# Kernel tuning notes

Measured on AMD Instinct MI355X. Metric: run time of the kernel, lower is better.

## Reference

```python
import jax, jax.numpy as jnp
import numpy as np

ANCHOR_LENGTHS = jnp.array([1., 2., 3., 4., 5., 7., 9.], dtype=jnp.float32)  # A = 7


def make_anchors_1d(Lf):
    # anchors [Lf*A, 2] in feature coords, matching torch make_anchors_1d
    centers = jnp.arange(Lf, dtype=jnp.float32) + 0.5          # [Lf]
    c = centers[:, None]                                        # [Lf,1]
    w = ANCHOR_LENGTHS[None, :]                                 # [1,A]
    start = c - 0.5 * w
    end = c + 0.5 * w
    return jnp.stack(jnp.broadcast_arrays(start, end), axis=-1).reshape(-1, 2)


def setup_inputs() -> dict:
    key = jax.random.key(0)
    ks = jax.random.split(key, 4)
    B, C, Lf, A = 8, 512, 16384, 7
    feat = jax.random.normal(ks[0], (B, C, Lf), dtype=jnp.float32)
    conv_w = jax.random.normal(ks[1], (C, C, 3), dtype=jnp.float32) * 0.02
    conv_b = jnp.zeros((C,), dtype=jnp.float32)
    obj_w = jax.random.normal(ks[2], (A, C, 1), dtype=jnp.float32) * 0.02
    obj_b = jnp.zeros((A,), dtype=jnp.float32)
    reg_w = jax.random.normal(ks[3], (A * 2, C, 1), dtype=jnp.float32) * 0.02
    reg_b = jnp.zeros((A * 2,), dtype=jnp.float32)
    return {"feat": feat, "conv_w": conv_w, "conv_b": conv_b,
            "obj_w": obj_w, "obj_b": obj_b, "reg_w": reg_w, "reg_b": reg_b}


def reference(feat, conv_w, conv_b, obj_w, obj_b, reg_w, reg_b):
    B, C, Lf = feat.shape
    A = obj_w.shape[0]
    # conv1d k=3 pad=1 (NCH layout), + bias, relu
    h = jax.lax.conv_general_dilated(
        feat, conv_w, window_strides=(1,), padding=((1, 1),),
        dimension_numbers=("NCH", "OIH", "NCH"))
    h = jax.nn.relu(h + conv_b[None, :, None])                  # [B,C,Lf]
    # 1x1 heads as channel contractions
    obj = jnp.einsum("bcl,ac->bla", h, obj_w[:, :, 0]) + obj_b  # [B,Lf,A]
    reg = jnp.einsum("bcl,oc->blo", h, reg_w[:, :, 0]) + reg_b  # [B,Lf,2A]
    obj = obj.reshape(B, Lf * A)                                # [B,N]
    reg = reg.reshape(B, Lf, A, 2).reshape(B, Lf * A, 2)        # [B,N,2]
    anchors = make_anchors_1d(Lf)                               # [N,2]
    return obj, reg, anchors
```

## Files before the change

### kernel.cpp

```cpp
#include <hip/hip_runtime.h>
#include <hip/hip_bf16.h>
#include <stdint.h>

typedef __attribute__((ext_vector_type(4))) float f32x4;
typedef __attribute__((ext_vector_type(16))) float f32x16;
typedef __attribute__((ext_vector_type(4))) int i32x4;
typedef __attribute__((ext_vector_type(8))) int i32x8;
typedef __attribute__((ext_vector_type(8))) short bh8;
typedef unsigned short u16;
typedef unsigned int u32;
typedef unsigned char u8;

#define B_    8
#define C_    512
#define LF    16384
#define KTOT  1536
#define SCL   0x7F7F7F7Fu

#define P4_BYTES ((size_t)4 * B_ * 21 * LF * 4)
#define W8_OFF   P4_BYTES

#define OBJ_OFF  0
#define REG_OFF  917504
#define ANC_OFF  2752512

__device__ __forceinline__ u16 f2bf(float f) {
    u32 u = __float_as_uint(f);
    return (u16)((u + 0x7FFFu + ((u >> 16) & 1u)) >> 16);
}
__device__ __forceinline__ u32 pk2bf(float lo, float hi) {
    u32 r;
    asm("v_cvt_pk_bf16_f32 %0, %1, %2" : "=v"(r) : "v"(lo), "v"(hi));
    return r;
}
__device__ __forceinline__ void gload16(const u8* g, u8* l) {
    __builtin_amdgcn_global_load_lds(
        (const __attribute__((address_space(1))) void*)g,
        (__attribute__((address_space(3))) void*)l, 16, 0, 0);
}

__global__ void k_cast_w(const float* __restrict__ cw, u8* __restrict__ W8) {
    int i = blockIdx.x * 256 + threadIdx.x;
    if (i >= C_ * KTOT / 2) return;
    int co = i / (KTOT / 2);
    int rr = (i % (KTOT / 2)) * 2;
    int t = rr / 512, q = rr % 512;
    int kc = q >> 6, cc = q & 63;
    int jl = (cc >> 4) ^ ((co >> 1) & 3);
    int ci = kc * 64 + jl * 16 + (cc & 15);
    float f0 = cw[(co * C_ + ci) * 3 + t];
    float f1 = cw[(co * C_ + ci + 1) * 3 + t];
    u32 pk = __builtin_amdgcn_cvt_pk_fp8_f32(f0, f1, 0, false);
    *(u16*)&W8[(size_t)co * KTOT + rr] = (u16)pk;
}

__global__ void k_anchors(float* __restrict__ out) {
    int l = blockIdx.x * 256 + threadIdx.x;
    if (l >= LF) return;
    const float AL[7] = {1.f, 2.f, 3.f, 4.f, 5.f, 7.f, 9.f};
    float c = (float)l + 0.5f;
    float* an = out + ANC_OFF + (size_t)l * 14;
#pragma unroll
    for (int a = 0; a < 7; ++a) {
        an[a * 2 + 0] = c - 0.5f * AL[a];
        an[a * 2 + 1] = c + 0.5f * AL[a];
    }
}

__global__ __launch_bounds__(256, 2) void k_conv_head(
    const float* __restrict__ feat, const u8* __restrict__ W8,
    const float* __restrict__ conv_b, const float* __restrict__ obj_w,
    const float* __restrict__ reg_w, float* __restrict__ P4) {
    __shared__ __align__(16) char smem[40960];
    u8* As3 = (u8*)smem;
    u8* Bs  = (u8*)(smem + 24576);
    u16* Hs = (u16*)smem;
    u16* Wp = (u16*)(smem + 32768);

    const int tid = threadIdx.x;
    const int lane = tid & 63, wave = tid >> 6;
    const int wm = wave >> 1, wn = wave & 1;
    const int g = lane >> 4, cL = lane & 15;
    const int r32 = lane & 31, hK = lane >> 5;

    const int wg = (blockIdx.x & 7) * 512 + (blockIdx.x >> 3);
    const int mt = wg & 3;
    const int l0 = ((wg >> 2) & 127) * 128;
    const int b  = wg >> 9;
    const int co0 = mt * 128;

    const int cg = tid & 15, lgrp = tid >> 4;

    f32x16 acc[2][2];
#pragma unroll
    for (int mi = 0; mi < 2; ++mi)
#pragma unroll
        for (int ni = 0; ni < 2; ++ni)
#pragma unroll
            for (int r = 0; r < 16; ++r) acc[mi][ni][r] = 0.f;

    for (int kc = 0; kc < 8; ++kc) {
        __syncthreads();
        {
            const float* fp = feat +
                ((size_t)(b * C_ + kc * 64 + cg * 4)) * LF + l0 + lgrp * 8;
            const int slog = cg >> 2;
            const int soff = (cg * 4) & 15;
#pragma unroll
            for (int h = 0; h < 2; ++h) {
                float4 v0 = *(const float4*)(fp + 0 * LF + h * 4);
                float4 v1 = *(const float4*)(fp + 1 * LF + h * 4);
                float4 v2 = *(const float4*)(fp + 2 * LF + h * 4);
                float4 v3 = *(const float4*)(fp + 3 * LF + h * 4);
#pragma unroll
                for (int e = 0; e < 4; ++e) {
                    const int r = 1 + lgrp * 8 + h * 4 + e;
                    u32 w0 = __builtin_amdgcn_cvt_pk_fp8_f32(
                        ((const float*)&v0)[e], ((const float*)&v1)[e], 0, false);
                    u32 w  = __builtin_amdgcn_cvt_pk_fp8_f32(
                        ((const float*)&v2)[e], ((const float*)&v3)[e], w0, true);
                    const int pc = ((slog ^ ((r >> 1) & 3)) * 16) + soff;
                    *(u32*)&Bs[r * 64 + pc] = w;
                }
            }
        }
        if (tid < 128) {
            const int ci2 = tid >> 1;
            const int rr = (tid & 1) ? 129 : 0;
            const int l = l0 + ((tid & 1) ? 128 : -1);
            float v = (l >= 0 && l < LF)
                          ? feat[((size_t)(b * C_ + kc * 64 + ci2)) * LF + l]
                          : 0.f;
            u32 p = __builtin_amdgcn_cvt_pk_fp8_f32(v, 0.f, 0, false);
            const int pc = (((ci2 >> 4) ^ ((rr >> 1) & 3)) * 16) + (ci2 & 15);
            Bs[rr * 64 + pc] = (u8)p;
        }
#pragma unroll
        for (int t = 0; t < 3; ++t)
#pragma unroll
            for (int p = 0; p < 2; ++p) {
                const int row = p * 64 + (tid >> 2);
                const int colB = (tid & 3) * 16;
                gload16(&W8[(size_t)(co0 + row) * KTOT + t * 512 + kc * 64 + colB],
                        &As3[t * 8192 + row * 64 + colB]);
            }
        __syncthreads();
#pragma unroll
        for (int t = 0; t < 3; ++t) {
            const u8* At = As3 + t * 8192;
            i32x8 af[2], bf[2];
#pragma unroll
            for (int mi = 0; mi < 2; ++mi) {
                const int row = wm * 64 + mi * 32 + r32;
                const int x = (row >> 1) & 3;
                i32x4 a0 = *(const i32x4*)&At[row * 64 + (((2 * hK) ^ x) * 16)];
                i32x4 a1 = *(const i32x4*)&At[row * 64 + (((2 * hK + 1) ^ x) * 16)];
                af[mi] = __builtin_shufflevector(a0, a1, 0, 1, 2, 3, 4, 5, 6, 7);
            }
#pragma unroll
            for (int ni = 0; ni < 2; ++ni) {
                const int row = wn * 64 + ni * 32 + r32 + t;
                const int x = (row >> 1) & 3;
                i32x4 b0 = *(const i32x4*)&Bs[row * 64 + (((2 * hK) ^ x) * 16)];
                i32x4 b1 = *(const i32x4*)&Bs[row * 64 + (((2 * hK + 1) ^ x) * 16)];
                bf[ni] = __builtin_shufflevector(b0, b1, 0, 1, 2, 3, 4, 5, 6, 7);
            }
#pragma unroll
            for (int mi = 0; mi < 2; ++mi)
#pragma unroll
                for (int ni = 0; ni < 2; ++ni)
                    acc[mi][ni] = __builtin_amdgcn_mfma_scale_f32_32x32x64_f8f6f4(
                        af[mi], bf[ni], acc[mi][ni], 0, 0, 0, SCL, 0, SCL);
        }
    }
    __syncthreads();

#pragma unroll
    for (int mi = 0; mi < 2; ++mi)
#pragma unroll
        for (int ni = 0; ni < 2; ++ni) {
            const int l_loc = wn * 64 + ni * 32 + r32;
            const int xw = (l_loc & 7) << 3;
#pragma unroll
            for (int q = 0; q < 4; ++q) {
                const int cb = wm * 64 + mi * 32 + q * 8 + 4 * hK;
                const float b0_ = conv_b[co0 + cb + 0];
                const float b1_ = conv_b[co0 + cb + 1];
                const float b2_ = conv_b[co0 + cb + 2];
                const float b3_ = conv_b[co0 + cb + 3];
                uint2 pk;
                pk.x = pk2bf(fmaxf(acc[mi][ni][q * 4 + 0] + b0_, 0.f),
                             fmaxf(acc[mi][ni][q * 4 + 1] + b1_, 0.f));
                pk.y = pk2bf(fmaxf(acc[mi][ni][q * 4 + 2] + b2_, 0.f),
                             fmaxf(acc[mi][ni][q * 4 + 3] + b3_, 0.f));
                *(uint2*)&Hs[l_loc * 128 + (cb ^ xw)] = pk;
            }
        }
#pragma unroll
    for (int it = 0; it < 4; ++it) {
        const int q = it * 256 + tid;
        const int a = q >> 5, c0 = (q & 31) * 4;
        float4 wv = {0.f, 0.f, 0.f, 0.f};
        if (a < 7)       wv = *(const float4*)&obj_w[a * C_ + co0 + c0];
        else if (a < 21) wv = *(const float4*)&reg_w[(a - 7) * C_ + co0 + c0];
        uint2 pk;
        pk.x = pk2bf(wv.x, wv.y);
        pk.y = pk2bf(wv.z, wv.w);
        *(uint2*)&Wp[a * 128 + (c0 ^ ((a & 7) << 3))] = pk;
    }
    __syncthreads();

    f32x4 hacc[2][2];
#pragma unroll
    for (int m = 0; m < 2; ++m)
#pragma unroll
        for (int n = 0; n < 2; ++n) hacc[m][n] = {0.f, 0.f, 0.f, 0.f};
    const int ln0 = wave * 32;
    const int swA = (cL & 7) << 3;
#pragma unroll
    for (int ks2 = 0; ks2 < 4; ++ks2) {
        const int ko = ks2 * 32 + g * 8;
        bh8 wa[2], hb[2];
        wa[0] = *(const bh8*)&Wp[cL * 128 + (ko ^ swA)];
        wa[1] = *(const bh8*)&Wp[(16 + cL) * 128 + (ko ^ swA)];
        hb[0] = *(const bh8*)&Hs[(ln0 + cL) * 128 + (ko ^ swA)];
        hb[1] = *(const bh8*)&Hs[(ln0 + 16 + cL) * 128 + (ko ^ swA)];
#pragma unroll
        for (int m = 0; m < 2; ++m)
#pragma unroll
            for (int n = 0; n < 2; ++n)
                hacc[m][n] = __builtin_amdgcn_mfma_f32_16x16x32_bf16(
                    wa[m], hb[n], hacc[m][n], 0, 0, 0);
    }
    float* P4base = P4 + ((size_t)(mt * B_ + b) * 21) * LF + l0;
#pragma unroll
    for (int m = 0; m < 2; ++m) {
        const int a0 = m * 16 + g * 4;
#pragma unroll
        for (int n = 0; n < 2; ++n) {
            const int l = ln0 + n * 16 + cL;
#pragma unroll
            for (int r = 0; r < 4; ++r) {
                const int a = a0 + r;
                if (a < 21) P4base[(size_t)a * LF + l] = hacc[m][n][r];
            }
        }
    }
}

__global__ void k_finalize(const float* __restrict__ P4, const float* __restrict__ obj_b,
                           const float* __restrict__ reg_b, float* __restrict__ out) {
    int gid = blockIdx.x * 256 + threadIdx.x;
    if (gid >= B_ * LF) return;
    int b = gid >> 14, l = gid & (LF - 1);
    float s[21];
#pragma unroll
    for (int a = 0; a < 21; ++a) {
        float v = 0.f;
#pragma unroll
        for (int m = 0; m < 4; ++m) v += P4[((size_t)(m * B_ + b) * 21 + a) * LF + l];
        s[a] = v;
    }
    float* op = out + OBJ_OFF + (size_t)b * (LF * 7) + (size_t)l * 7;
#pragma unroll
    for (int a = 0; a < 7; ++a) op[a] = s[a] + obj_b[a];
    float* rp = out + REG_OFF + (size_t)b * (LF * 14) + (size_t)l * 14;
#pragma unroll
    for (int o = 0; o < 14; ++o) rp[o] = s[7 + o] + reg_b[o];
}

extern "C" void kernel_launch(void* const* d_in, const int* in_sizes, int n_in,
                              void* d_out, int out_size, void* d_ws, size_t ws_size,
                              hipStream_t stream) {
    const float* feat   = (const float*)d_in[0];
    const float* conv_w = (const float*)d_in[1];
    const float* conv_b = (const float*)d_in[2];
    const float* obj_w  = (const float*)d_in[3];
    const float* obj_b  = (const float*)d_in[4];
    const float* reg_w  = (const float*)d_in[5];
    const float* reg_b  = (const float*)d_in[6];
    char* ws = (char*)d_ws;
    float* P4 = (float*)ws;
    u8* W8    = (u8*)(ws + W8_OFF);
    float* out = (float*)d_out;

    k_cast_w<<<1536, 256, 0, stream>>>(conv_w, W8);
    k_anchors<<<64, 256, 0, stream>>>(out);
    k_conv_head<<<4096, 256, 0, stream>>>(feat, W8, conv_b, obj_w, reg_w, P4);
    k_finalize<<<(B_ * LF + 255) / 256, 256, 0, stream>>>(P4, obj_b, reg_b, out);
}
```

Baseline: 236.7 us.

## Double K-chunk to 128 channels, stage one tap of weights at a time, raise occupancy

The conv GEMM main loop now processes 128 input channels per outer step instead of 64, with the weight layout and XOR swizzle widened to 128-byte rows (8-way swizzle). Weights are staged one kernel tap at a time into a single 16KB buffer rather than all three taps at once, and launch bounds go from 2 to 4 blocks per CU. The aim is fewer outer iterations and higher occupancy to hide latency, at the cost of more barriers per channel chunk and heavier register use from eight float4 feature loads at a time.

```diff
diff --git a/kernel.cpp b/kernel.cpp
--- a/kernel.cpp
+++ b/kernel.cpp
@@ -24,10 +24,6 @@
 #define REG_OFF  917504
 #define ANC_OFF  2752512
 
-__device__ __forceinline__ u16 f2bf(float f) {
-    u32 u = __float_as_uint(f);
-    return (u16)((u + 0x7FFFu + ((u >> 16) & 1u)) >> 16);
-}
 __device__ __forceinline__ u32 pk2bf(float lo, float hi) {
     u32 r;
     asm("v_cvt_pk_bf16_f32 %0, %1, %2" : "=v"(r) : "v"(lo), "v"(hi));
@@ -38,6 +34,7 @@
         (const __attribute__((address_space(1))) void*)g,
         (__attribute__((address_space(3))) void*)l, 16, 0, 0);
 }
+__device__ __forceinline__ int xr7(int r) { return (r & 7) ^ ((r >> 3) & 7); }
 
 __global__ void k_cast_w(const float* __restrict__ cw, u8* __restrict__ W8) {
     int i = blockIdx.x * 256 + threadIdx.x;
@@ -45,9 +42,10 @@
     int co = i / (KTOT / 2);
     int rr = (i % (KTOT / 2)) * 2;
     int t = rr / 512, q = rr % 512;
-    int kc = q >> 6, cc = q & 63;
-    int jl = (cc >> 4) ^ ((co >> 1) & 3);
-    int ci = kc * 64 + jl * 16 + (cc & 15);
+    int kcp = q >> 7, pb = q & 127;
+    int sp = pb >> 4;
+    int sl = sp ^ xr7(co);
+    int ci = kcp * 128 + sl * 16 + (pb & 15);
     float f0 = cw[(co * C_ + ci) * 3 + t];
     float f1 = cw[(co * C_ + ci + 1) * 3 + t];
     u32 pk = __builtin_amdgcn_cvt_pk_fp8_f32(f0, f1, 0, false);
@@ -67,13 +65,13 @@
     }
 }
 
-__global__ __launch_bounds__(256, 2) void k_conv_head(
+__global__ __launch_bounds__(256, 4) void k_conv_head(
     const float* __restrict__ feat, const u8* __restrict__ W8,
     const float* __restrict__ conv_b, const float* __restrict__ obj_w,
     const float* __restrict__ reg_w, float* __restrict__ P4) {
     __shared__ __align__(16) char smem[40960];
-    u8* As3 = (u8*)smem;
-    u8* Bs  = (u8*)(smem + 24576);
+    u8* As = (u8*)smem;
+    u8* Bs = (u8*)(smem + 16384);
     u16* Hs = (u16*)smem;
     u16* Wp = (u16*)(smem + 32768);
 
@@ -99,81 +97,85 @@
 #pragma unroll
             for (int r = 0; r < 16; ++r) acc[mi][ni][r] = 0.f;
 
-    for (int kc = 0; kc < 8; ++kc) {
-        __syncthreads();
+    for (int kcp = 0; kcp < 4; ++kcp) {
         {
             const float* fp = feat +
-                ((size_t)(b * C_ + kc * 64 + cg * 4)) * LF + l0 + lgrp * 8;
-            const int slog = cg >> 2;
-            const int soff = (cg * 4) & 15;
+                ((size_t)(b * C_ + kcp * 128 + cg * 8)) * LF + l0 + lgrp * 8;
+            const int sl = cg >> 1;
+            const int half = (cg & 1) * 8;
 #pragma unroll
             for (int h = 0; h < 2; ++h) {
-                float4 v0 = *(const float4*)(fp + 0 * LF + h * 4);
-                float4 v1 = *(const float4*)(fp + 1 * LF + h * 4);
-                float4 v2 = *(const float4*)(fp + 2 * LF + h * 4);
-                float4 v3 = *(const float4*)(fp + 3 * LF + h * 4);
+                float4 v[8];
+#pragma unroll
+                for (int j = 0; j < 8; ++j)
+                    v[j] = *(const float4*)(fp + (size_t)j * LF + h * 4);
 #pragma unroll
                 for (int e = 0; e < 4; ++e) {
                     const int r = 1 + lgrp * 8 + h * 4 + e;
                     u32 w0 = __builtin_amdgcn_cvt_pk_fp8_f32(
-                        ((const float*)&v0)[e], ((const float*)&v1)[e], 0, false);
-                    u32 w  = __builtin_amdgcn_cvt_pk_fp8_f32(
-                        ((const float*)&v2)[e], ((const float*)&v3)[e], w0, true);
-                    const int pc = ((slog ^ ((r >> 1) & 3)) * 16) + soff;
-                    *(u32*)&Bs[r * 64 + pc] = w;
+                        ((const float*)&v[0])[e], ((const float*)&v[1])[e], 0, false);
+                    w0 = __builtin_amdgcn_cvt_pk_fp8_f32(
+                        ((const float*)&v[2])[e], ((const float*)&v[3])[e], w0, true);
+                    u32 w1 = __builtin_amdgcn_cvt_pk_fp8_f32(
+                        ((const float*)&v[4])[e], ((const float*)&v[5])[e], 0, false);
+                    w1 = __builtin_amdgcn_cvt_pk_fp8_f32(
+                        ((const float*)&v[6])[e], ((const float*)&v[7])[e], w1, true);
+                    uint2 pk; pk.x = w0; pk.y = w1;
+                    *(uint2*)&Bs[r * 128 + ((sl ^ xr7(r)) * 16) + half] = pk;
                 }
             }
         }
         if (tid < 128) {
-            const int ci2 = tid >> 1;
-            const int rr = (tid & 1) ? 129 : 0;
-            const int l = l0 + ((tid & 1) ? 128 : -1);
-            float v = (l >= 0 && l < LF)
-                          ? feat[((size_t)(b * C_ + kc * 64 + ci2)) * LF + l]
-                          : 0.f;
-            u32 p = __builtin_amdgcn_cvt_pk_fp8_f32(v, 0.f, 0, false);
-            const int pc = (((ci2 >> 4) ^ ((rr >> 1) & 3)) * 16) + (ci2 & 15);
-            Bs[rr * 64 + pc] = (u8)p;
-        }
-#pragma unroll
-        for (int t = 0; t < 3; ++t)
-#pragma unroll
-            for (int p = 0; p < 2; ++p) {
-                const int row = p * 64 + (tid >> 2);
-                const int colB = (tid & 3) * 16;
-                gload16(&W8[(size_t)(co0 + row) * KTOT + t * 512 + kc * 64 + colB],
-                        &As3[t * 8192 + row * 64 + colB]);
-            }
-        __syncthreads();
+#pragma unroll
+            for (int hh = 0; hh < 2; ++hh) {
+                const int rr = hh ? 129 : 0;
+                const int l = l0 + (hh ? 128 : -1);
+                float v = (l >= 0 && l < LF)
+                              ? feat[((size_t)(b * C_ + kcp * 128 + tid)) * LF + l]
+                              : 0.f;
+                u32 p = __builtin_amdgcn_cvt_pk_fp8_f32(v, 0.f, 0, false);
+                Bs[rr * 128 + (((tid >> 4) ^ xr7(rr)) * 16) + (tid & 15)] = (u8)p;
+            }
+        }
 #pragma unroll
         for (int t = 0; t < 3; ++t) {
-            const u8* At = As3 + t * 8192;
-            i32x8 af[2], bf[2];
-#pragma unroll
-            for (int mi = 0; mi < 2; ++mi) {
-                const int row = wm * 64 + mi * 32 + r32;
-                const int x = (row >> 1) & 3;
-                i32x4 a0 = *(const i32x4*)&At[row * 64 + (((2 * hK) ^ x) * 16)];
-                i32x4 a1 = *(const i32x4*)&At[row * 64 + (((2 * hK + 1) ^ x) * 16)];
-                af[mi] = __builtin_shufflevector(a0, a1, 0, 1, 2, 3, 4, 5, 6, 7);
-            }
-#pragma unroll
-            for (int ni = 0; ni < 2; ++ni) {
-                const int row = wn * 64 + ni * 32 + r32 + t;
-                const int x = (row >> 1) & 3;
-                i32x4 b0 = *(const i32x4*)&Bs[row * 64 + (((2 * hK) ^ x) * 16)];
-                i32x4 b1 = *(const i32x4*)&Bs[row * 64 + (((2 * hK + 1) ^ x) * 16)];
-                bf[ni] = __builtin_shufflevector(b0, b1, 0, 1, 2, 3, 4, 5, 6, 7);
-            }
-#pragma unroll
-            for (int mi = 0; mi < 2; ++mi)
-#pragma unroll
-                for (int ni = 0; ni < 2; ++ni)
-                    acc[mi][ni] = __builtin_amdgcn_mfma_scale_f32_32x32x64_f8f6f4(
-                        af[mi], bf[ni], acc[mi][ni], 0, 0, 0, SCL, 0, SCL);
-        }
-    }
-    __syncthreads();
+#pragma unroll
+            for (int q = 0; q < 4; ++q) {
+                const int flat = q * 256 + tid;
+                const int row = flat >> 3, colB = (flat & 7) * 16;
+                gload16(&W8[(size_t)(co0 + row) * KTOT + t * 512 + kcp * 128 + colB],
+                        &As[row * 128 + colB]);
+            }
+            __syncthreads();
+#pragma unroll
+            for (int kk = 0; kk < 2; ++kk) {
+                i32x8 af[2], bf[2];
+#pragma unroll
+                for (int mi = 0; mi < 2; ++mi) {
+                    const int row = wm * 64 + mi * 32 + r32;
+                    const int xa = xr7(row);
+                    i32x4 a0 = *(const i32x4*)&As[row * 128 + (((4 * kk + 2 * hK) ^ xa) * 16)];
+                    i32x4 a1 = *(const i32x4*)&As[row * 128 + (((4 * kk + 2 * hK + 1) ^ xa) * 16)];
+                    af[mi] = __builtin_shufflevector(a0, a1, 0, 1, 2, 3, 4, 5, 6, 7);
+                }
+#pragma unroll
+                for (int ni = 0; ni < 2; ++ni) {
+                    const int row = wn * 64 + ni * 32 + r32 + t;
+                    const int xb = xr7(row);
+                    i32x4 b0 = *(const i32x4*)&Bs[row * 128 + (((4 * kk + 2 * hK) ^ xb) * 16)];
+                    i32x4 b1 = *(const i32x4*)&Bs[row * 128 + (((4 * kk + 2 * hK + 1) ^ xb) * 16)];
+                    bf[ni] = __builtin_shufflevector(b0, b1, 0, 1, 2, 3, 4, 5, 6, 7);
+                }
+#pragma unroll
+                for (int mi = 0; mi < 2; ++mi)
+#pragma unroll
+                    for (int ni = 0; ni < 2; ++ni)
+                        acc[mi][ni] = __builtin_amdgcn_mfma_scale_f32_32x32x64_f8f6f4(
+                            af[mi], bf[ni], acc[mi][ni], 0, 0, 0, SCL, 0, SCL);
+            }
+            __syncthreads();
+        }
+    }
 
 #pragma unroll
     for (int mi = 0; mi < 2; ++mi)
```

New measurement: 464.3 us. 96.1% more time.
